# Kernel optimization log

Hardware: AMD Instinct MI355X
Metric: run time of the kernel (lower is better)

The kernel has to match this reference:

```python
import jax, jax.numpy as jnp
import numpy as np

N_NODES = 50000
EPS = 1e-16
NEG_SLOPE = 0.2


def _gat_conv(x, src, dst, W, a_src, a_dst, bias, heads, out_c, concat, n):
    # Linear transform: [N, heads, out_c]
    h = (x @ W).reshape(n, heads, out_c)
    # Per-node attention logits (split form of PyG's 'a' vector)
    al_src = jnp.einsum('nhc,hc->nh', h, a_src)  # [N, H]
    al_dst = jnp.einsum('nhc,hc->nh', h, a_dst)  # [N, H]
    # Edge-wise scores, softmax over incoming edges of each destination
    e = jax.nn.leaky_relu(al_src[src] + al_dst[dst], NEG_SLOPE)  # [E, H]
    m = jax.ops.segment_max(e, dst, num_segments=n)              # [N, H]
    ex = jnp.exp(e - m[dst])
    s = jax.ops.segment_sum(ex, dst, num_segments=n)             # [N, H]
    alpha = ex / (s[dst] + EPS)                                  # [E, H]
    # Attention-weighted scatter-aggregate of source features
    out = jax.ops.segment_sum(h[src] * alpha[:, :, None], dst, num_segments=n)
    if concat:
        out = out.reshape(n, heads * out_c)
    else:
        out = out.mean(axis=1)
    return out + bias


def _add_self_loops(edge_index, n):
    loop = jnp.arange(n, dtype=edge_index.dtype)
    src = jnp.concatenate([edge_index[0], loop])
    dst = jnp.concatenate([edge_index[1], loop])
    return src, dst


def setup_inputs() -> dict:
    key = jax.random.key(0)
    ks = jax.random.split(key, 10)
    n, e = N_NODES, 640000
    x = jax.random.normal(ks[0], (n, 128), dtype=jnp.float32)
    edge_index = jax.random.randint(ks[1], (2, e), 0, n, dtype=jnp.int64)
    sc = 0.1
    return {
        'x': x,
        'edge_index': edge_index,
        'W1': jax.random.normal(ks[2], (128, 256), dtype=jnp.float32) * sc,
        'a1_src': jax.random.normal(ks[3], (8, 32), dtype=jnp.float32) * sc,
        'a1_dst': jax.random.normal(ks[4], (8, 32), dtype=jnp.float32) * sc,
        'b1': jax.random.normal(ks[5], (256,), dtype=jnp.float32) * sc,
        'W2': jax.random.normal(ks[6], (256, 64), dtype=jnp.float32) * sc,
        'a2_src': jax.random.normal(ks[7], (1, 64), dtype=jnp.float32) * sc,
        'a2_dst': jax.random.normal(ks[8], (1, 64), dtype=jnp.float32) * sc,
        'b2': jax.random.normal(ks[9], (64,), dtype=jnp.float32) * sc,
    }


def reference(x, edge_index, W1, a1_src, a1_dst, b1, W2, a2_src, a2_dst, b2):
    n = x.shape[0]
    src, dst = _add_self_loops(edge_index, n)  # PyG GATConv add_self_loops=True
    # Dropouts are identity in eval mode.
    h = _gat_conv(x, src, dst, W1, a1_src, a1_dst, b1, heads=8, out_c=32, concat=True, n=n)
    h = jax.nn.elu(h)
    out = _gat_conv(h, src, dst, W2, a2_src, a2_dst, b2, heads=1, out_c=64, concat=False, n=n)
    return out
```

## Files before the change

kernel.cpp:

```cpp
#include <hip/hip_runtime.h>


static __device__ __forceinline__ float lrelu(float x) { return x > 0.f ? x : 0.2f * x; }

__global__ void count_deg(const int* __restrict__ dstv, int* __restrict__ deg, int E) {
  int e = blockIdx.x * blockDim.x + threadIdx.x;
  if (e < E) atomicAdd(&deg[dstv[e]], 1);
}

__global__ void scan_partial(const int* __restrict__ deg, int* __restrict__ off,
                             int* __restrict__ bsum, int n) {
  int tid = threadIdx.x;
  int i = blockIdx.x * 256 + tid;
  int v = (i < n) ? deg[i] : 0;
  int lane = tid & 63, w = tid >> 6;
  int sv = v;
#pragma unroll
  for (int o = 1; o < 64; o <<= 1) {
    int t = __shfl_up(sv, o);
    if (lane >= o) sv += t;
  }
  __shared__ int ws[4];
  if (lane == 63) ws[w] = sv;
  __syncthreads();
  int add = 0;
  for (int j = 0; j < w; ++j) add += ws[j];
  sv += add;
  if (i < n) off[i + 1] = sv;
  if (tid == 255) bsum[blockIdx.x] = sv;
}

__global__ void scan_bsum(int* __restrict__ bsum, int* __restrict__ off, int nb) {
  int tid = threadIdx.x;
  int v = (tid < nb) ? bsum[tid] : 0;
  int lane = tid & 63, w = tid >> 6;
  int sv = v;
#pragma unroll
  for (int o = 1; o < 64; o <<= 1) {
    int t = __shfl_up(sv, o);
    if (lane >= o) sv += t;
  }
  __shared__ int ws[4];
  if (lane == 63) ws[w] = sv;
  __syncthreads();
  int add = 0;
  for (int j = 0; j < w; ++j) add += ws[j];
  sv += add;
  if (tid < nb) bsum[tid] = sv - v;
  if (tid == 0) off[0] = 0;
}

__global__ void add_carry(const int* __restrict__ deg, int* __restrict__ off,
                          const int* __restrict__ bsum, int* __restrict__ cur, int n) {
  int i = blockIdx.x * 256 + threadIdx.x;
  if (i < n) {
    int o = off[i + 1] + bsum[blockIdx.x];
    off[i + 1] = o;
    cur[i] = o - deg[i];
  }
}

__global__ void fill_csr(const int* __restrict__ srcv, const int* __restrict__ dstv,
                         int* __restrict__ cur, int* __restrict__ csr, int E) {
  int e = blockIdx.x * blockDim.x + threadIdx.x;
  if (e < E) {
    int p = atomicAdd(&cur[dstv[e]], 1);
    csr[p] = srcv[e];
  }
}

__global__ __launch_bounds__(256) void gemm1(const float* __restrict__ x, const float* __restrict__ W,
                                             float* __restrict__ h, int n) {
  __shared__ float xs[32][64];
  __shared__ float Ws[32][256];
  int tid = threadIdx.x;
  int tc = tid & 31;
  int tr = tid >> 5;
  int lr = tid & 63, lj = tid >> 6;
  int r0 = blockIdx.x * 64;

  float acc[8][8];
#pragma unroll
  for (int r = 0; r < 8; ++r)
#pragma unroll
    for (int j = 0; j < 8; ++j) acc[r][j] = 0.f;

  for (int k0 = 0; k0 < 128; k0 += 32) {
    __syncthreads();
    {
      int rr = r0 + lr;
      float4 v0 = {0, 0, 0, 0}, v1 = {0, 0, 0, 0};
      if (rr < n) {
        const float* p = x + (size_t)rr * 128 + k0 + lj * 8;
        v0 = *(const float4*)p;
        v1 = *(const float4*)(p + 4);
      }
      int kk = lj * 8;
      xs[kk + 0][lr] = v0.x; xs[kk + 1][lr] = v0.y; xs[kk + 2][lr] = v0.z; xs[kk + 3][lr] = v0.w;
      xs[kk + 4][lr] = v1.x; xs[kk + 5][lr] = v1.y; xs[kk + 6][lr] = v1.z; xs[kk + 7][lr] = v1.w;
    }
    {
      const float4* src = (const float4*)(W + (size_t)k0 * 256);
      float4* dst = (float4*)&Ws[0][0];
#pragma unroll
      for (int i = tid; i < 2048; i += 256) dst[i] = src[i];
    }
    __syncthreads();
#pragma unroll 4
    for (int k = 0; k < 32; ++k) {
      float xv[8];
      *(float4*)&xv[0] = *(const float4*)&xs[k][tr * 8];
      *(float4*)&xv[4] = *(const float4*)&xs[k][tr * 8 + 4];
      float wv[8];
#pragma unroll
      for (int j = 0; j < 8; ++j) wv[j] = Ws[k][tc + 32 * j];
#pragma unroll
      for (int r = 0; r < 8; ++r)
#pragma unroll
        for (int j = 0; j < 8; ++j) acc[r][j] = fmaf(xv[r], wv[j], acc[r][j]);
    }
  }
#pragma unroll
  for (int r = 0; r < 8; ++r) {
    int row = r0 + tr * 8 + r;
    if (row < n) {
#pragma unroll
      for (int j = 0; j < 8; ++j) h[(size_t)row * 256 + tc + 32 * j] = acc[r][j];
    }
  }
}

__global__ __launch_bounds__(256) void gemm2(const float* __restrict__ xin, const float* __restrict__ W,
                                             float* __restrict__ h, int n) {
  __shared__ float xs[32][128];
  __shared__ float Ws[32][64];
  int tid = threadIdx.x;
  int tc = tid & 15;
  int tr = tid >> 4;
  int r0 = blockIdx.x * 128;

  float acc[8][4];
#pragma unroll
  for (int r = 0; r < 8; ++r)
#pragma unroll
    for (int j = 0; j < 4; ++j) acc[r][j] = 0.f;

  for (int k0 = 0; k0 < 256; k0 += 32) {
    __syncthreads();
#pragma unroll
    for (int idx = tid; idx < 1024; idx += 256) {
      int r = idx & 127, q = idx >> 7;
      int rr = r0 + r;
      float4 v = {0, 0, 0, 0};
      if (rr < n) v = *(const float4*)(xin + (size_t)rr * 256 + k0 + q * 4);
      int kk = q * 4;
      xs[kk + 0][r] = v.x; xs[kk + 1][r] = v.y; xs[kk + 2][r] = v.z; xs[kk + 3][r] = v.w;
    }
    {
      const float4* src = (const float4*)(W + (size_t)k0 * 64);
      float4* dst = (float4*)&Ws[0][0];
#pragma unroll
      for (int i = tid; i < 512; i += 256) dst[i] = src[i];
    }
    __syncthreads();
#pragma unroll 4
    for (int k = 0; k < 32; ++k) {
      float xv[8];
      *(float4*)&xv[0] = *(const float4*)&xs[k][tr * 8];
      *(float4*)&xv[4] = *(const float4*)&xs[k][tr * 8 + 4];
      float wv[4];
#pragma unroll
      for (int j = 0; j < 4; ++j) wv[j] = Ws[k][tc + 16 * j];
#pragma unroll
      for (int r = 0; r < 8; ++r)
#pragma unroll
        for (int j = 0; j < 4; ++j) acc[r][j] = fmaf(xv[r], wv[j], acc[r][j]);
    }
  }
#pragma unroll
  for (int r = 0; r < 8; ++r) {
    int row = r0 + tr * 8 + r;
    if (row < n) {
#pragma unroll
      for (int j = 0; j < 4; ++j) h[(size_t)row * 64 + tc + 16 * j] = acc[r][j];
    }
  }
}

__global__ __launch_bounds__(256) void logits1(const float* __restrict__ h, const float* __restrict__ as,
                                               const float* __restrict__ ad, float* __restrict__ als,
                                               float* __restrict__ ald, int n) {
  int node = blockIdx.x * 4 + (threadIdx.x >> 6);
  int lane = threadIdx.x & 63;
  if (node >= n) return;
  float4 v = *(const float4*)&h[(size_t)node * 256 + lane * 4];
  float4 cs = *(const float4*)&as[lane * 4];
  float4 cd = *(const float4*)&ad[lane * 4];
  float ps = v.x * cs.x + v.y * cs.y + v.z * cs.z + v.w * cs.w;
  float pd = v.x * cd.x + v.y * cd.y + v.z * cd.z + v.w * cd.w;
#pragma unroll
  for (int o = 1; o < 8; o <<= 1) {
    ps += __shfl_xor(ps, o);
    pd += __shfl_xor(pd, o);
  }
  if ((lane & 7) == 0) {
    int head = lane >> 3;
    als[node * 8 + head] = ps;
    ald[node * 8 + head] = pd;
  }
}

__global__ __launch_bounds__(256) void logits2(const float* __restrict__ h, const float* __restrict__ as,
                                               const float* __restrict__ ad, float* __restrict__ als,
                                               float* __restrict__ ald, int n) {
  int node = blockIdx.x * 4 + (threadIdx.x >> 6);
  int lane = threadIdx.x & 63;
  if (node >= n) return;
  float v = h[(size_t)node * 64 + lane];
  float ps = v * as[lane];
  float pd = v * ad[lane];
#pragma unroll
  for (int o = 1; o < 64; o <<= 1) {
    ps += __shfl_xor(ps, o);
    pd += __shfl_xor(pd, o);
  }
  if (lane == 0) {
    als[node] = ps;
    ald[node] = pd;
  }
}

__global__ __launch_bounds__(256) void agg1(const float* __restrict__ h, const float* __restrict__ al_src,
                                            const float* __restrict__ al_dst, const int* __restrict__ off,
                                            const int* __restrict__ csr, const float* __restrict__ bias,
                                            float* __restrict__ outp, int n) {
  int d = blockIdx.x;
  int tid = threadIdx.x;
  int head = tid >> 5;
  float ad = al_dst[d * 8 + head];
  float w0 = expf(lrelu(al_src[d * 8 + head] + ad));
  float acc = w0 * h[(size_t)d * 256 + tid];
  float wsum = w0;
  int beg = off[d], end = off[d + 1];
  int i = beg;
  for (; i + 1 < end; i += 2) {
    int s0 = csr[i], s1 = csr[i + 1];
    float a0 = al_src[s0 * 8 + head];
    float a1 = al_src[s1 * 8 + head];
    float h0 = h[(size_t)s0 * 256 + tid];
    float h1 = h[(size_t)s1 * 256 + tid];
    float wa = expf(lrelu(a0 + ad));
    float wb = expf(lrelu(a1 + ad));
    acc = fmaf(wa, h0, acc);
    acc = fmaf(wb, h1, acc);
    wsum += wa + wb;
  }
  if (i < end) {
    int s = csr[i];
    float w = expf(lrelu(al_src[s * 8 + head] + ad));
    acc = fmaf(w, h[(size_t)s * 256 + tid], acc);
    wsum += w;
  }
  float v = acc / (wsum + 1e-16f) + bias[tid];
  outp[(size_t)d * 256 + tid] = v > 0.f ? v : expm1f(v);
}

__global__ __launch_bounds__(256) void agg2(const float* __restrict__ h, const float* __restrict__ al_src,
                                            const float* __restrict__ al_dst, const int* __restrict__ off,
                                            const int* __restrict__ csr, const float* __restrict__ bias,
                                            float* __restrict__ outp, int n) {
  int d = blockIdx.x * 4 + (threadIdx.x >> 6);
  int c = threadIdx.x & 63;
  if (d >= n) return;
  float ad = al_dst[d];
  float w0 = expf(lrelu(al_src[d] + ad));
  float acc = w0 * h[(size_t)d * 64 + c];
  float wsum = w0;
  int beg = off[d], end = off[d + 1];
  int i = beg;
  for (; i + 1 < end; i += 2) {
    int s0 = csr[i], s1 = csr[i + 1];
    float a0 = al_src[s0];
    float a1 = al_src[s1];
    float h0 = h[(size_t)s0 * 64 + c];
    float h1 = h[(size_t)s1 * 64 + c];
    float wa = expf(lrelu(a0 + ad));
    float wb = expf(lrelu(a1 + ad));
    acc = fmaf(wa, h0, acc);
    acc = fmaf(wb, h1, acc);
    wsum += wa + wb;
  }
  if (i < end) {
    int s = csr[i];
    float w = expf(lrelu(al_src[s] + ad));
    acc = fmaf(w, h[(size_t)s * 64 + c], acc);
    wsum += w;
  }
  outp[(size_t)d * 64 + c] = acc / (wsum + 1e-16f) + bias[c];
}

extern "C" void kernel_launch(void* const* d_in, const int* in_sizes, int n_in,
                              void* d_out, int out_size, void* d_ws, size_t ws_size,
                              hipStream_t stream) {
  const float* x  = (const float*)d_in[0];
  const int* ei   = (const int*)d_in[1];
  const float* W1 = (const float*)d_in[2];
  const float* a1s = (const float*)d_in[3];
  const float* a1d = (const float*)d_in[4];
  const float* b1  = (const float*)d_in[5];
  const float* W2  = (const float*)d_in[6];
  const float* a2s = (const float*)d_in[7];
  const float* a2d = (const float*)d_in[8];
  const float* b2  = (const float*)d_in[9];
  float* outp = (float*)d_out;

  int n = in_sizes[0] / 128;
  int E = in_sizes[1] / 2;
  const int* srcv = ei;
  const int* dstv = ei + E;

  char* wsb = (char*)d_ws;
  size_t p = 0;
  auto alloc = [&](size_t bytes) -> char* {
    char* r = wsb + p;
    p += (bytes + 511) & ~size_t(511);
    return r;
  };
  int* deg  = (int*)alloc((size_t)n * 4);
  int* off  = (int*)alloc(((size_t)n + 1) * 4);
  int* cur  = (int*)alloc((size_t)n * 4);
  int* bsum = (int*)alloc(1024);
  int* csr  = (int*)alloc((size_t)E * 4);
  float* h1   = (float*)alloc((size_t)n * 256 * 4);
  float* al1s = (float*)alloc((size_t)n * 8 * 4);
  float* al1d = (float*)alloc((size_t)n * 8 * 4);
  float* o1   = (float*)alloc((size_t)n * 256 * 4);
  float* h2   = (float*)alloc((size_t)n * 64 * 4);
  float* al2s = (float*)alloc((size_t)n * 4);
  float* al2d = (float*)alloc((size_t)n * 4);
  (void)ws_size;

  hipMemsetAsync(deg, 0, (size_t)n * 4, stream);
  int eb = (E + 255) / 256;
  int nb = (n + 255) / 256;
  count_deg<<<eb, 256, 0, stream>>>(dstv, deg, E);
  scan_partial<<<nb, 256, 0, stream>>>(deg, off, bsum, n);
  scan_bsum<<<1, 256, 0, stream>>>(bsum, off, nb);
  add_carry<<<nb, 256, 0, stream>>>(deg, off, bsum, cur, n);
  fill_csr<<<eb, 256, 0, stream>>>(srcv, dstv, cur, csr, E);

  gemm1<<<(n + 63) / 64, 256, 0, stream>>>(x, W1, h1, n);
  logits1<<<(n + 3) / 4, 256, 0, stream>>>(h1, a1s, a1d, al1s, al1d, n);
  agg1<<<n, 256, 0, stream>>>(h1, al1s, al1d, off, csr, b1, o1, n);
  gemm2<<<(n + 127) / 128, 256, 0, stream>>>(o1, W2, h2, n);
  logits2<<<(n + 3) / 4, 256, 0, stream>>>(h2, a2s, a2d, al2s, al2d, n);
  agg2<<<(n + 3) / 4, 256, 0, stream>>>(h2, al2s, al2d, off, csr, b2, outp, n);
}
```

Measured before the change: 445.1 us.

## Precompute per-edge attention weights and vectorize layer-1 aggregation with float4 per wave

Edge attention weights exp(leaky_relu(src+dst)) are now computed once per edge and head in separate kernels, using a new CSR-ordered destination array, instead of inside the aggregation loops. Layer-1 aggregation now maps one 64-lane wavefront per destination node with float4 loads, replacing one 256-thread block per node. This removes redundant exp work and gives wider memory accesses. In exchange it adds two launches plus writes and reads of E*8 and E alpha floats and the extra csr_dst array.

```diff
diff --git a/kernel.cpp b/kernel.cpp
--- a/kernel.cpp
+++ b/kernel.cpp
@@ -61,11 +61,14 @@
 }
 
 __global__ void fill_csr(const int* __restrict__ srcv, const int* __restrict__ dstv,
-                         int* __restrict__ cur, int* __restrict__ csr, int E) {
+                         int* __restrict__ cur, int* __restrict__ csr,
+                         int* __restrict__ csr_dst, int E) {
   int e = blockIdx.x * blockDim.x + threadIdx.x;
   if (e < E) {
-    int p = atomicAdd(&cur[dstv[e]], 1);
+    int d = dstv[e];
+    int p = atomicAdd(&cur[d], 1);
     csr[p] = srcv[e];
+    csr_dst[p] = d;
   }
 }
 
@@ -230,69 +233,96 @@
   }
 }
 
-__global__ __launch_bounds__(256) void agg1(const float* __restrict__ h, const float* __restrict__ al_src,
-                                            const float* __restrict__ al_dst, const int* __restrict__ off,
-                                            const int* __restrict__ csr, const float* __restrict__ bias,
-                                            float* __restrict__ outp, int n) {
-  int d = blockIdx.x;
-  int tid = threadIdx.x;
-  int head = tid >> 5;
-  float ad = al_dst[d * 8 + head];
-  float w0 = expf(lrelu(al_src[d * 8 + head] + ad));
-  float acc = w0 * h[(size_t)d * 256 + tid];
+__global__ __launch_bounds__(256) void alpha1_k(const float* __restrict__ als, const float* __restrict__ ald,
+                                                const int* __restrict__ csr, const int* __restrict__ csr_dst,
+                                                float* __restrict__ alpha, int E) {
+  int idx = blockIdx.x * 256 + threadIdx.x;
+  if (idx >= E * 8) return;
+  int p = idx >> 3, hd = idx & 7;
+  int s = csr[p], d = csr_dst[p];
+  alpha[idx] = expf(lrelu(als[s * 8 + hd] + ald[d * 8 + hd]));
+}
+
+__global__ __launch_bounds__(256) void alpha2_k(const float* __restrict__ als, const float* __restrict__ ald,
+                                                const int* __restrict__ csr, const int* __restrict__ csr_dst,
+                                                float* __restrict__ alpha, int E) {
+  int p = blockIdx.x * 256 + threadIdx.x;
+  if (p >= E) return;
+  alpha[p] = expf(lrelu(als[csr[p]] + ald[csr_dst[p]]));
+}
+
+__global__ __launch_bounds__(256) void agg1(const float* __restrict__ h, const float* __restrict__ alpha,
+                                            const float* __restrict__ als, const float* __restrict__ ald,
+                                            const int* __restrict__ off, const int* __restrict__ csr,
+                                            const float* __restrict__ bias, float* __restrict__ outp, int n) {
+  int d = blockIdx.x * 4 + (threadIdx.x >> 6);
+  if (d >= n) return;
+  int lane = threadIdx.x & 63;
+  int head = lane >> 3;
+  float w0 = expf(lrelu(als[d * 8 + head] + ald[d * 8 + head]));
+  float4 hv = *(const float4*)&h[(size_t)d * 256 + lane * 4];
+  float4 acc;
+  acc.x = w0 * hv.x; acc.y = w0 * hv.y; acc.z = w0 * hv.z; acc.w = w0 * hv.w;
   float wsum = w0;
   int beg = off[d], end = off[d + 1];
   int i = beg;
   for (; i + 1 < end; i += 2) {
     int s0 = csr[i], s1 = csr[i + 1];
-    float a0 = al_src[s0 * 8 + head];
-    float a1 = al_src[s1 * 8 + head];
-    float h0 = h[(size_t)s0 * 256 + tid];
-    float h1 = h[(size_t)s1 * 256 + tid];
-    float wa = expf(lrelu(a0 + ad));
-    float wb = expf(lrelu(a1 + ad));
-    acc = fmaf(wa, h0, acc);
-    acc = fmaf(wb, h1, acc);
+    float wa = alpha[(size_t)i * 8 + head];
+    float wb = alpha[(size_t)(i + 1) * 8 + head];
+    float4 h0 = *(const float4*)&h[(size_t)s0 * 256 + lane * 4];
+    float4 h1 = *(const float4*)&h[(size_t)s1 * 256 + lane * 4];
+    acc.x = fmaf(wa, h0.x, acc.x); acc.y = fmaf(wa, h0.y, acc.y);
+    acc.z = fmaf(wa, h0.z, acc.z); acc.w = fmaf(wa, h0.w, acc.w);
+    acc.x = fmaf(wb, h1.x, acc.x); acc.y = fmaf(wb, h1.y, acc.y);
+    acc.z = fmaf(wb, h1.z, acc.z); acc.w = fmaf(wb, h1.w, acc.w);
     wsum += wa + wb;
   }
   if (i < end) {
     int s = csr[i];
-    float w = expf(lrelu(al_src[s * 8 + head] + ad));
-    acc = fmaf(w, h[(size_t)s * 256 + tid], acc);
+    float w = alpha[(size_t)i * 8 + head];
+    float4 h0 = *(const float4*)&h[(size_t)s * 256 + lane * 4];
+    acc.x = fmaf(w, h0.x, acc.x); acc.y = fmaf(w, h0.y, acc.y);
+    acc.z = fmaf(w, h0.z, acc.z); acc.w = fmaf(w, h0.w, acc.w);
     wsum += w;
   }
-  float v = acc / (wsum + 1e-16f) + bias[tid];
-  outp[(size_t)d * 256 + tid] = v > 0.f ? v : expm1f(v);
-}
-
-__global__ __launch_bounds__(256) void agg2(const float* __restrict__ h, const float* __restrict__ al_src,
-                                            const float* __restrict__ al_dst, const int* __restrict__ off,
-                                            const int* __restrict__ csr, const float* __restrict__ bias,
-                                            float* __restrict__ outp, int n) {
+  float inv = 1.f / (wsum + 1e-16f);
+  float4 b = *(const float4*)&bias[lane * 4];
+  float4 o;
+  o.x = acc.x * inv + b.x; o.y = acc.y * inv + b.y;
+  o.z = acc.z * inv + b.z; o.w = acc.w * inv + b.w;
+  o.x = o.x > 0.f ? o.x : expm1f(o.x);
+  o.y = o.y > 0.f ? o.y : expm1f(o.y);
+  o.z = o.z > 0.f ? o.z : expm1f(o.z);
+  o.w = o.w > 0.f ? o.w : expm1f(o.w);
+  *(float4*)&outp[(size_t)d * 256 + lane * 4] = o;
+}
+
+__global__ __launch_bounds__(256) void agg2(const float* __restrict__ h, const float* __restrict__ alpha,
+                                            const float* __restrict__ als, const float* __restrict__ ald,
+                                            const int* __restrict__ off, const int* __restrict__ csr,
+                                            const float* __restrict__ bias, float* __restrict__ outp, int n) {
   int d = blockIdx.x * 4 + (threadIdx.x >> 6);
+  if (d >= n) return;
   int c = threadIdx.x & 63;
-  if (d >= n) return;
-  float ad = al_dst[d];
-  float w0 = expf(lrelu(al_src[d] + ad));
+  float w0 = expf(lrelu(als[d] + ald[d]));
   float acc = w0 * h[(size_t)d * 64 + c];
   float wsum = w0;
   int beg = off[d], end = off[d + 1];
   int i = beg;
   for (; i + 1 < end; i += 2) {
     int s0 = csr[i], s1 = csr[i + 1];
-    float a0 = al_src[s0];
-    float a1 = al_src[s1];
+    float wa = alpha[i];
+    float wb = alpha[i + 1];
     float h0 = h[(size_t)s0 * 64 + c];
     float h1 = h[(size_t)s1 * 64 + c];
-    float wa = expf(lrelu(a0 + ad));
-    float wb = expf(lrelu(a1 + ad));
     acc = fmaf(wa, h0, acc);
     acc = fmaf(wb, h1, acc);
     wsum += wa + wb;
   }
   if (i < end) {
     int s = csr[i];
-    float w = expf(lrelu(al_src[s] + ad));
+    float w = alpha[i];
     acc = fmaf(w, h[(size_t)s * 64 + c], acc);
     wsum += w;
   }
@@ -331,6 +361,7 @@
   int* cur  = (int*)alloc((size_t)n * 4);
   int* bsum = (int*)alloc(1024);
   int* csr  = (int*)alloc((size_t)E * 4);
+  int* csrd = (int*)alloc((size_t)E * 4);
   float* h1   = (float*)alloc((size_t)n * 256 * 4);
   float* al1s = (float*)alloc((size_t)n * 8 * 4);
   float* al1d = (float*)alloc((size_t)n * 8 * 4);
@@ -338,6 +369,8 @@
   float* h2   = (float*)alloc((size_t)n * 64 * 4);
   float* al2s = (float*)alloc((size_t)n * 4);
   float* al2d = (float*)alloc((size_t)n * 4);
+  float* alp1 = (float*)alloc((size_t)E * 8 * 4);
+  float* alp2 = (float*)alloc((size_t)E * 4);
   (void)ws_size;
 
   hipMemsetAsync(deg, 0, (size_t)n * 4, stream);
@@ -347,12 +380,14 @@
   scan_partial<<<nb, 256, 0, stream>>>(deg, off, bsum, n);
   scan_bsum<<<1, 256, 0, stream>>>(bsum, off, nb);
   add_carry<<<nb, 256, 0, stream>>>(deg, off, bsum, cur, n);
-  fill_csr<<<eb, 256, 0, stream>>>(srcv, dstv, cur, csr, E);
+  fill_csr<<<eb, 256, 0, stream>>>(srcv, dstv, cur, csr, csrd, E);
 
   gemm1<<<(n + 63) / 64, 256, 0, stream>>>(x, W1, h1, n);
   logits1<<<(n + 3) / 4, 256, 0, stream>>>(h1, a1s, a1d, al1s, al1d, n);
-  agg1<<<n, 256, 0, stream>>>(h1, al1s, al1d, off, csr, b1, o1, n);
+  alpha1_k<<<(E * 8 + 255) / 256, 256, 0, stream>>>(al1s, al1d, csr, csrd, alp1, E);
+  agg1<<<(n + 3) / 4, 256, 0, stream>>>(h1, alp1, al1s, al1d, off, csr, b1, o1, n);
   gemm2<<<(n + 127) / 128, 256, 0, stream>>>(o1, W2, h2, n);
   logits2<<<(n + 3) / 4, 256, 0, stream>>>(h2, a2s, a2d, al2s, al2d, n);
-  agg2<<<(n + 3) / 4, 256, 0, stream>>>(h2, al2s, al2d, off, csr, b2, outp, n);
-}
+  alpha2_k<<<eb, 256, 0, stream>>>(al2s, al2d, csr, csrd, alp2, E);
+  agg2<<<(n + 3) / 4, 256, 0, stream>>>(h2, alp2, al2s, al2d, off, csr, b2, outp, n);
+}
```

After: 436.8 us. No clear change (-1.9%).
